# Optimization experiments

Hardware: AMD Instinct MI355X
Metric: run time of the kernel (lower is better)

The kernel has to match this reference:

```python
import jax, jax.numpy as jnp
import numpy as np

B, L, N = 512, 512, 128


def setup_inputs() -> dict:
    key = jax.random.key(0)
    k1, k2, k3, k4 = jax.random.split(key, 4)
    emission = jax.random.normal(k1, (B, L, N), dtype=jnp.float32)
    target = jax.random.randint(k2, (B, L), 0, N, dtype=jnp.int32)
    mask = jnp.ones((B, L), dtype=jnp.float32)
    # params: uniform(-0.1, 0.1) as in reset_parameters
    start_trans = jax.random.uniform(k3, (N,), minval=-0.1, maxval=0.1, dtype=jnp.float32)
    trans = jax.random.uniform(k4, (N, N), minval=-0.1, maxval=0.1, dtype=jnp.float32)
    return {"emission": emission, "target": target, "mask": mask,
            "start_trans": start_trans, "trans": trans}


def _normalizer(emission, mask, start_trans, trans):
    # scores: [B, N]
    scores0 = start_trans + emission[:, 0]
    em_t = jnp.swapaxes(emission, 0, 1)[1:]          # [L-1, B, N]
    m_t = jnp.swapaxes(mask, 0, 1)[1:, :, None]      # [L-1, B, 1]

    def step(scores, xs):
        em_i, m_i = xs
        nxt = jax.nn.logsumexp(scores[:, :, None] + trans[None], axis=1) + em_i
        nxt = m_i * nxt + (1.0 - m_i) * scores
        return nxt, None

    final, _ = jax.lax.scan(step, scores0, (em_t, m_t))
    return jax.nn.logsumexp(final, axis=1)            # [B]


def _path_score(emission, target, mask, start_trans, trans):
    # mask*next + (1-mask)*scores == scores + mask*increment -> fully vectorizable
    b = jnp.arange(emission.shape[0])
    t0 = target[:, 0]
    s0 = start_trans[t0] + emission[b, 0, t0]                         # [B]
    prev, cur = target[:, :-1], target[:, 1:]                         # [B, L-1]
    em_gather = jnp.take_along_axis(emission[:, 1:], cur[:, :, None], axis=2)[..., 0]
    inc = trans[prev, cur] + em_gather                                # [B, L-1]
    return s0 + jnp.sum(mask[:, 1:] * inc, axis=1)                    # [B]


def reference(emission, target, mask, start_trans, trans):
    path_scores = _path_score(emission, target, mask, start_trans, trans)
    normalizer = _normalizer(emission, mask, start_trans, trans)
    return jnp.mean(normalizer - path_scores)
```

## Files before the change

kernel.cpp:

```cpp
#include <hip/hip_runtime.h>

#define B_ 512
#define L_ 512
#define N_ 128
#define TM 256
#define C_BIAS 3.0f

typedef _Float16 h2_t __attribute__((ext_vector_type(2)));
typedef _Float16 h8_t __attribute__((ext_vector_type(8)));
typedef float    f4_t __attribute__((ext_vector_type(4)));

#define DPP_STEP_MAX(v, ctrl)                                                   \
    {                                                                           \
        int _t = __builtin_amdgcn_update_dpp(__float_as_int(v),                 \
                    __float_as_int(v), ctrl, 0xf, 0xf, false);                  \
        v = fmaxf(v, __int_as_float(_t));                                       \
    }
#define DPP_STEP_ADD(v, ctrl)                                                   \
    {                                                                           \
        int _t = __builtin_amdgcn_update_dpp(__float_as_int(v),                 \
                    __float_as_int(v), ctrl, 0xf, 0xf, false);                  \
        v = v + __int_as_float(_t);                                             \
    }

__device__ __forceinline__ float wave_max(float v) {
    DPP_STEP_MAX(v, 0xB1);
    DPP_STEP_MAX(v, 0x4E);
    DPP_STEP_MAX(v, 0x141);
    DPP_STEP_MAX(v, 0x140);
    DPP_STEP_MAX(v, 0x142);
    DPP_STEP_MAX(v, 0x143);
    return __int_as_float(__builtin_amdgcn_readlane(__float_as_int(v), 63));
}
__device__ __forceinline__ float wave_sum(float v) {
    DPP_STEP_ADD(v, 0xB1);
    DPP_STEP_ADD(v, 0x4E);
    DPP_STEP_ADD(v, 0x141);
    DPP_STEP_ADD(v, 0x140);
    DPP_STEP_ADD(v, 0x142);
    DPP_STEP_ADD(v, 0x143);
    return __int_as_float(__builtin_amdgcn_readlane(__float_as_int(v), 63));
}

#define CHAIN4(qv, BT)                                                          \
    f4_t qv = __builtin_amdgcn_mfma_f32_16x16x32_f16(A0, BT[0], z, 0, 0, 0);    \
    qv = __builtin_amdgcn_mfma_f32_16x16x32_f16(A1, BT[1], qv, 0, 0, 0);        \
    qv = __builtin_amdgcn_mfma_f32_16x16x32_f16(A2, BT[2], qv, 0, 0, 0);        \
    qv = __builtin_amdgcn_mfma_f32_16x16x32_f16(A3, BT[3], qv, 0, 0, 0);

__global__ __launch_bounds__(64, 1) void norm_kernel(
    const float* __restrict__ em, const int* __restrict__ tg,
    const float* __restrict__ mask, const float* __restrict__ st,
    const float* __restrict__ trans,
    float* __restrict__ alpha, float* __restrict__ beta,
    float* __restrict__ pathf, float* __restrict__ pathb)
{
    __shared__ __align__(16) _Float16 Eh[128];
    __shared__ float Mlds[TM];

    const int l  = threadIdx.x;
    const int c  = l & 15;
    const int h  = l >> 4;
    const int s0 = 32 * h + c;
    const int s1 = s0 + 16;
    const bool hb0 = (h & 1) != 0;
    const bool hb1 = (h & 2) != 0;
    const int b  = blockIdx.x >> 1;
    const int bw = blockIdx.x & 1;
    const size_t base = (size_t)b * L_ * N_;
    const int bL = b * L_;

    if (bw == 0) {
        float pacc = 0.f;
        for (int t = 1 + l; t < TM; t += 64) {
            int cur  = tg[bL + t];
            int prev = tg[bL + t - 1];
            pacc += mask[bL + t] * (trans[prev * N_ + cur] + em[base + (size_t)t * N_ + cur]);
        }
        pacc = wave_sum(pacc);
        if (l == 0) {
            int t0 = tg[bL];
            pathf[b] = pacc + st[t0] + em[base + t0];
        }

#pragma unroll
        for (int k = 0; k < 4; ++k) Mlds[l + 64 * k] = mask[bL + l + 64 * k];

        h8_t Bf[8][4];
#pragma unroll
        for (int jt = 0; jt < 8; ++jt)
#pragma unroll
            for (int ks = 0; ks < 4; ++ks) {
                h8_t f;
#pragma unroll
                for (int e = 0; e < 8; ++e)
                    f[e] = (_Float16)__expf(trans[(32 * ks + 8 * h + e) * N_ + 16 * jt + c]);
                Bf[jt][ks] = f;
            }

        float ns0 = st[s0] + em[base + s0];
        float ns1 = st[s1] + em[base + s1];
        float Mprev = wave_max(fmaxf(ns0, ns1));
        Eh[s0] = (_Float16)__expf(ns0 - Mprev - C_BIAS);
        Eh[s1] = (_Float16)__expf(ns1 - Mprev - C_BIAS);

        float pa0 = em[base + (size_t)1 * N_ + s0], pb0 = em[base + (size_t)1 * N_ + s1];
        float pa1 = em[base + (size_t)2 * N_ + s0], pb1 = em[base + (size_t)2 * N_ + s1];
        float pa2 = em[base + (size_t)3 * N_ + s0], pb2 = em[base + (size_t)3 * N_ + s1];
        float pa3 = em[base + (size_t)4 * N_ + s0], pb3 = em[base + (size_t)4 * N_ + s1];

        auto step = [&](int t, float& sa, float& sb) {
            float emv0 = sa, emv1 = sb;
            int tpf = t + 4; if (tpf > TM - 1) tpf = TM - 1;
            sa = em[base + (size_t)tpf * N_ + s0];
            sb = em[base + (size_t)tpf * N_ + s1];
            float mk = Mlds[t];

            float mx = wave_max(fmaxf(ns0, ns1));

            const _Float16* Eb = (const _Float16*)Eh;
            h8_t A0 = *(const h8_t*)(Eb + 8 * h);
            h8_t A1 = *(const h8_t*)(Eb + 32 + 8 * h);
            h8_t A2 = *(const h8_t*)(Eb + 64 + 8 * h);
            h8_t A3 = *(const h8_t*)(Eb + 96 + 8 * h);

            f4_t z = {0.f, 0.f, 0.f, 0.f};
            CHAIN4(q0, Bf[0]) CHAIN4(q1, Bf[1]) CHAIN4(q2, Bf[2]) CHAIN4(q3, Bf[3])
            CHAIN4(q4, Bf[4]) CHAIN4(q5, Bf[5]) CHAIN4(q6, Bf[6]) CHAIN4(q7, Bf[7])

            float sv0 = hb1 ? (hb0 ? q6[0] : q4[0]) : (hb0 ? q2[0] : q0[0]);
            float sv1 = hb1 ? (hb0 ? q7[0] : q5[0]) : (hb0 ? q3[0] : q1[0]);

            float badd = Mprev + C_BIAS;
            float nxt0 = __logf(sv0) + badd + emv0;
            float nxt1 = __logf(sv1) + badd + emv1;
            float im = 1.f - mk;
            ns0 = mk * nxt0 + im * ns0;
            ns1 = mk * nxt1 + im * ns1;

            Mprev = mx;
            Eh[s0] = (_Float16)__expf(ns0 - mx - C_BIAS);
            Eh[s1] = (_Float16)__expf(ns1 - mx - C_BIAS);
        };

        for (int tt = 1; tt + 3 < TM; tt += 4) {
            step(tt    , pa0, pb0);
            step(tt + 1, pa1, pb1);
            step(tt + 2, pa2, pb2);
            step(tt + 3, pa3, pb3);
        }
        step(TM - 3, pa0, pb0);
        step(TM - 2, pa1, pb1);
        step(TM - 1, pa2, pb2);

        alpha[b * N_ + s0] = ns0;
        alpha[b * N_ + s1] = ns1;
    } else {
        float pacc = 0.f;
        for (int t = TM + l; t < L_; t += 64) {
            int cur  = tg[bL + t];
            int prev = tg[bL + t - 1];
            pacc += mask[bL + t] * (trans[prev * N_ + cur] + em[base + (size_t)t * N_ + cur]);
        }
        pacc = wave_sum(pacc);
        if (l == 0) pathb[b] = pacc;

#pragma unroll
        for (int k = 0; k < 4; ++k) Mlds[l + 64 * k] = mask[bL + TM + l + 64 * k];

        h8_t Bf[8][4];
#pragma unroll
        for (int it = 0; it < 8; ++it)
#pragma unroll
            for (int ks = 0; ks < 4; ++ks) {
                const float* p = trans + (size_t)(16 * it + c) * N_ + 32 * ks + 8 * h;
                float4 q0 = *(const float4*)p;
                float4 q1 = *(const float4*)(p + 4);
                h8_t f;
                f[0] = (_Float16)__expf(q0.x); f[1] = (_Float16)__expf(q0.y);
                f[2] = (_Float16)__expf(q0.z); f[3] = (_Float16)__expf(q0.w);
                f[4] = (_Float16)__expf(q1.x); f[5] = (_Float16)__expf(q1.y);
                f[6] = (_Float16)__expf(q1.z); f[7] = (_Float16)__expf(q1.w);
                Bf[it][ks] = f;
            }

        float b0 = 0.f, b1 = 0.f;
        float v0 = em[base + (size_t)(L_ - 1) * N_ + s0];
        float v1 = em[base + (size_t)(L_ - 1) * N_ + s1];
        float Mprev = wave_max(fmaxf(v0, v1));
        Eh[s0] = (_Float16)__expf(v0 - Mprev - C_BIAS);
        Eh[s1] = (_Float16)__expf(v1 - Mprev - C_BIAS);

        float pa0 = em[base + (size_t)510 * N_ + s0], pb0 = em[base + (size_t)510 * N_ + s1];
        float pa1 = em[base + (size_t)509 * N_ + s0], pb1 = em[base + (size_t)509 * N_ + s1];
        float pa2 = em[base + (size_t)508 * N_ + s0], pb2 = em[base + (size_t)508 * N_ + s1];
        float pa3 = em[base + (size_t)507 * N_ + s0], pb3 = em[base + (size_t)507 * N_ + s1];

        auto step = [&](int t, float& sa, float& sb) {
            float emt0 = sa, emt1 = sb;
            int tpf = t - 4; if (tpf < TM - 1) tpf = TM - 1;
            sa = em[base + (size_t)tpf * N_ + s0];
            sb = em[base + (size_t)tpf * N_ + s1];
            float mk = Mlds[t + 1 - TM];

            float mx = wave_max(fmaxf(v0, v1));

            const _Float16* Fb = (const _Float16*)Eh;
            h8_t A0 = *(const h8_t*)(Fb + 8 * h);
            h8_t A1 = *(const h8_t*)(Fb + 32 + 8 * h);
            h8_t A2 = *(const h8_t*)(Fb + 64 + 8 * h);
            h8_t A3 = *(const h8_t*)(Fb + 96 + 8 * h);

            f4_t z = {0.f, 0.f, 0.f, 0.f};
            CHAIN4(q0, Bf[0]) CHAIN4(q1, Bf[1]) CHAIN4(q2, Bf[2]) CHAIN4(q3, Bf[3])
            CHAIN4(q4, Bf[4]) CHAIN4(q5, Bf[5]) CHAIN4(q6, Bf[6]) CHAIN4(q7, Bf[7])

            float sv0 = hb1 ? (hb0 ? q6[0] : q4[0]) : (hb0 ? q2[0] : q0[0]);
            float sv1 = hb1 ? (hb0 ? q7[0] : q5[0]) : (hb0 ? q3[0] : q1[0]);

            float badd = Mprev + C_BIAS;
            float upd0 = __logf(sv0) + badd;
            float upd1 = __logf(sv1) + badd;
            float im = 1.f - mk;
            b0 = mk * upd0 + im * b0;
            b1 = mk * upd1 + im * b1;

            v0 = b0 + emt0;
            v1 = b1 + emt1;
            Mprev = mx;
            Eh[s0] = (_Float16)__expf(v0 - mx - C_BIAS);
            Eh[s1] = (_Float16)__expf(v1 - mx - C_BIAS);
        };

        for (int tt = 510; tt >= 258; tt -= 4) {
            step(tt    , pa0, pb0);
            step(tt - 1, pa1, pb1);
            step(tt - 2, pa2, pb2);
            step(tt - 3, pa3, pb3);
        }

        beta[b * N_ + s0] = b0;
        beta[b * N_ + s1] = b1;
    }
}

__global__ __launch_bounds__(64) void zres_kernel(
    const float* __restrict__ alpha, const float* __restrict__ beta,
    const float* __restrict__ pathf, const float* __restrict__ pathb,
    float* __restrict__ zres)
{
    const int l = threadIdx.x;
    const int b = blockIdx.x;
    float2 av = *(const float2*)(alpha + b * N_ + 2 * l);
    float2 bv = *(const float2*)(beta  + b * N_ + 2 * l);
    float v0 = av.x + bv.x;
    float v1 = av.y + bv.y;
    float m = wave_max(fmaxf(v0, v1));
    float s = wave_sum(__expf(v0 - m) + __expf(v1 - m));
    if (l == 0) zres[b] = m + __logf(s) - pathf[b] - pathb[b];
}

__global__ __launch_bounds__(64) void mean_kernel(
    const float* __restrict__ zres, float* __restrict__ out)
{
    const int l = threadIdx.x;
    const float4* z4 = (const float4*)zres;
    float4 a = z4[2 * l];
    float4 c = z4[2 * l + 1];
    float acc = ((a.x + a.y) + (a.z + a.w)) + ((c.x + c.y) + (c.z + c.w));
    acc = wave_sum(acc);
    if (l == 0) out[0] = acc * (1.0f / (float)B_);
}

extern "C" void kernel_launch(void* const* d_in, const int* in_sizes, int n_in,
                              void* d_out, int out_size, void* d_ws, size_t ws_size,
                              hipStream_t stream) {
    const float* emission    = (const float*)d_in[0];
    const int*   target      = (const int*)  d_in[1];
    const float* mask        = (const float*)d_in[2];
    const float* start_trans = (const float*)d_in[3];
    const float* trans       = (const float*)d_in[4];
    float* out = (float*)d_out;

    float* ws_f  = (float*)d_ws;
    float* alpha = ws_f;
    float* beta  = ws_f + B_ * N_;
    float* pathf = ws_f + 2 * B_ * N_;
    float* pathb = ws_f + 2 * B_ * N_ + B_;
    float* zres  = ws_f + 2 * B_ * N_ + 2 * B_;

    norm_kernel<<<2 * B_, 64, 0, stream>>>(emission, target, mask, start_trans,
                                           trans, alpha, beta, pathf, pathb);
    zres_kernel<<<B_, 64, 0, stream>>>(alpha, beta, pathf, pathb, zres);
    mean_kernel<<<1, 64, 0, stream>>>(zres, out);
}
```

Measured before the change: 307.7 us.

## Switch CRF recurrence matmul from fp16 MFMA chains to scaled FP8 MFMA

Replaces the four chained fp16 16x16x32 MFMAs per output tile with a single scaled 16x16x128 FP8 (e4m3) MFMA. The exp(trans) matrix and the per-step exp-scores vector are quantized to FP8 with unit scales. This shortens the serial per-timestep latency chain of the latency-bound recurrence, and also shrinks the register-held B fragments and the LDS vector. The cost is much lower precision in the exponentiated scores (3 mantissa bits, and small values get flushed or become subnormal), which risks accuracy error in the normalizer over 511 steps.

```diff
diff --git a/kernel.cpp b/kernel.cpp
--- a/kernel.cpp
+++ b/kernel.cpp
@@ -6,9 +6,8 @@
 #define TM 256
 #define C_BIAS 3.0f
 
-typedef _Float16 h2_t __attribute__((ext_vector_type(2)));
-typedef _Float16 h8_t __attribute__((ext_vector_type(8)));
-typedef float    f4_t __attribute__((ext_vector_type(4)));
+typedef float f4_t __attribute__((ext_vector_type(4)));
+typedef int   v8i_t __attribute__((ext_vector_type(8)));
 
 #define DPP_STEP_MAX(v, ctrl)                                                   \
     {                                                                           \
@@ -42,11 +41,44 @@
     return __int_as_float(__builtin_amdgcn_readlane(__float_as_int(v), 63));
 }
 
-#define CHAIN4(qv, BT)                                                          \
-    f4_t qv = __builtin_amdgcn_mfma_f32_16x16x32_f16(A0, BT[0], z, 0, 0, 0);    \
-    qv = __builtin_amdgcn_mfma_f32_16x16x32_f16(A1, BT[1], qv, 0, 0, 0);        \
-    qv = __builtin_amdgcn_mfma_f32_16x16x32_f16(A2, BT[2], qv, 0, 0, 0);        \
-    qv = __builtin_amdgcn_mfma_f32_16x16x32_f16(A3, BT[3], qv, 0, 0, 0);
+#if __has_builtin(__builtin_amdgcn_cvt_pk_fp8_f32)
+__device__ __forceinline__ unsigned fp8_pair(float a, float b) {
+    return (unsigned)__builtin_amdgcn_cvt_pk_fp8_f32(a, b, 0, false);
+}
+__device__ __forceinline__ unsigned fp8_quad(float a, float b, float c, float d) {
+    int lo = __builtin_amdgcn_cvt_pk_fp8_f32(a, b, 0, false);
+    return (unsigned)__builtin_amdgcn_cvt_pk_fp8_f32(c, d, lo, true);
+}
+#else
+__device__ __forceinline__ unsigned char f32_e4m3(float v) {
+    if (!(v > 0.f)) return 0;
+    if (v >= 448.f) return 0x7E;
+    if (v < 0.015625f) {
+        int m = (int)(v * 512.f + 0.5f);
+        return (unsigned char)m;
+    }
+    union { float f; unsigned u; } x; x.f = v;
+    unsigned u = x.u;
+    unsigned lsb = (u >> 20) & 1;
+    u += 0x0007FFFF + lsb;
+    int e = (int)((u >> 23) & 255) - 127 + 7;
+    unsigned m = (u >> 20) & 7;
+    if (e > 15) return 0x7E;
+    return (unsigned char)((e << 3) | m);
+}
+__device__ __forceinline__ unsigned fp8_pair(float a, float b) {
+    return (unsigned)f32_e4m3(a) | ((unsigned)f32_e4m3(b) << 8);
+}
+__device__ __forceinline__ unsigned fp8_quad(float a, float b, float c, float d) {
+    return fp8_pair(a, b) | (fp8_pair(c, d) << 16);
+}
+#endif
+
+#define SCALE_ONE 0x7F7F7F7F
+
+#define MXMFMA(qv, bt)                                                          \
+    f4_t qv = __builtin_amdgcn_mfma_scale_f32_16x16x128_f8f6f4(                 \
+        Afrag, bt, z, 0, 0, 0, SCALE_ONE, 0, SCALE_ONE);
 
 __global__ __launch_bounds__(64, 1) void norm_kernel(
     const float* __restrict__ em, const int* __restrict__ tg,
@@ -55,7 +87,7 @@
     float* __restrict__ alpha, float* __restrict__ beta,
     float* __restrict__ pathf, float* __restrict__ pathb)
 {
-    __shared__ __align__(16) _Float16 Eh[128];
+    __shared__ __align__(32) unsigned char Eh[128];
     __shared__ float Mlds[TM];
 
     const int l  = threadIdx.x;
@@ -86,23 +118,30 @@
 #pragma unroll
         for (int k = 0; k < 4; ++k) Mlds[l + 64 * k] = mask[bL + l + 64 * k];
 
-        h8_t Bf[8][4];
-#pragma unroll
-        for (int jt = 0; jt < 8; ++jt)
-#pragma unroll
-            for (int ks = 0; ks < 4; ++ks) {
-                h8_t f;
-#pragma unroll
-                for (int e = 0; e < 8; ++e)
-                    f[e] = (_Float16)__expf(trans[(32 * ks + 8 * h + e) * N_ + 16 * jt + c]);
-                Bf[jt][ks] = f;
+        v8i_t Bf[8];
+#pragma unroll
+        for (int jt = 0; jt < 8; ++jt) {
+            v8i_t bb;
+#pragma unroll
+            for (int dd = 0; dd < 8; ++dd) {
+                const float* p = trans + (size_t)(32 * h + 4 * dd) * N_ + 16 * jt + c;
+                float f0 = __expf(p[0]);
+                float f1 = __expf(p[N_]);
+                float f2 = __expf(p[2 * N_]);
+                float f3 = __expf(p[3 * N_]);
+                bb[dd] = (int)fp8_quad(f0, f1, f2, f3);
             }
+            Bf[jt] = bb;
+        }
 
         float ns0 = st[s0] + em[base + s0];
         float ns1 = st[s1] + em[base + s1];
         float Mprev = wave_max(fmaxf(ns0, ns1));
-        Eh[s0] = (_Float16)__expf(ns0 - Mprev - C_BIAS);
-        Eh[s1] = (_Float16)__expf(ns1 - Mprev - C_BIAS);
+        {
+            unsigned p = fp8_pair(__expf(ns0 - Mprev - C_BIAS), __expf(ns1 - Mprev - C_BIAS));
+            Eh[s0] = (unsigned char)(p & 0xFF);
+            Eh[s1] = (unsigned char)((p >> 8) & 0xFF);
+        }
 
         float pa0 = em[base + (size_t)1 * N_ + s0], pb0 = em[base + (size_t)1 * N_ + s1];
         float pa1 = em[base + (size_t)2 * N_ + s0], pb1 = em[base + (size_t)2 * N_ + s1];
@@ -118,15 +157,11 @@
 
             float mx = wave_max(fmaxf(ns0, ns1));
 
-            const _Float16* Eb = (const _Float16*)Eh;
-            h8_t A0 = *(const h8_t*)(Eb + 8 * h);
-            h8_t A1 = *(const h8_t*)(Eb + 32 + 8 * h);
-            h8_t A2 = *(const h8_t*)(Eb + 64 + 8 * h);
-            h8_t A3 = *(const h8_t*)(Eb + 96 + 8 * h);
+            v8i_t Afrag = *(const v8i_t*)(Eh + 32 * h);
 
             f4_t z = {0.f, 0.f, 0.f, 0.f};
-            CHAIN4(q0, Bf[0]) CHAIN4(q1, Bf[1]) CHAIN4(q2, Bf[2]) CHAIN4(q3, Bf[3])
-            CHAIN4(q4, Bf[4]) CHAIN4(q5, Bf[5]) CHAIN4(q6, Bf[6]) CHAIN4(q7, Bf[7])
+            MXMFMA(q0, Bf[0]) MXMFMA(q1, Bf[1]) MXMFMA(q2, Bf[2]) MXMFMA(q3, Bf[3])
+            MXMFMA(q4, Bf[4]) MXMFMA(q5, Bf[5]) MXMFMA(q6, Bf[6]) MXMFMA(q7, Bf[7])
 
             float sv0 = hb1 ? (hb0 ? q6[0] : q4[0]) : (hb0 ? q2[0] : q0[0]);
             float sv1 = hb1 ? (hb0 ? q7[0] : q5[0]) : (hb0 ? q3[0] : q1[0]);
@@ -139,8 +174,9 @@
             ns1 = mk * nxt1 + im * ns1;
 
             Mprev = mx;
-            Eh[s0] = (_Float16)__expf(ns0 - mx - C_BIAS);
-            Eh[s1] = (_Float16)__expf(ns1 - mx - C_BIAS);
+            unsigned p = fp8_pair(__expf(ns0 - mx - C_BIAS), __expf(ns1 - mx - C_BIAS));
+            Eh[s0] = (unsigned char)(p & 0xFF);
+            Eh[s1] = (unsigned char)((p >> 8) & 0xFF);
         };
 
         for (int tt = 1; tt + 3 < TM; tt += 4) {
@@ -168,28 +204,27 @@
 #pragma unroll
         for (int k = 0; k < 4; ++k) Mlds[l + 64 * k] = mask[bL + TM + l + 64 * k];
 
-        h8_t Bf[8][4];
-#pragma unroll
-        for (int it = 0; it < 8; ++it)
-#pragma unroll
-            for (int ks = 0; ks < 4; ++ks) {
-                const float* p = trans + (size_t)(16 * it + c) * N_ + 32 * ks + 8 * h;
-                float4 q0 = *(const float4*)p;
-                float4 q1 = *(const float4*)(p + 4);
-                h8_t f;
-                f[0] = (_Float16)__expf(q0.x); f[1] = (_Float16)__expf(q0.y);
-                f[2] = (_Float16)__expf(q0.z); f[3] = (_Float16)__expf(q0.w);
-                f[4] = (_Float16)__expf(q1.x); f[5] = (_Float16)__expf(q1.y);
-                f[6] = (_Float16)__expf(q1.z); f[7] = (_Float16)__expf(q1.w);
-                Bf[it][ks] = f;
+        v8i_t Bf[8];
+#pragma unroll
+        for (int it = 0; it < 8; ++it) {
+            v8i_t bb;
+#pragma unroll
+            for (int dd = 0; dd < 8; ++dd) {
+                float4 q = *(const float4*)(trans + (size_t)(16 * it + c) * N_ + 32 * h + 4 * dd);
+                bb[dd] = (int)fp8_quad(__expf(q.x), __expf(q.y), __expf(q.z), __expf(q.w));
             }
+            Bf[it] = bb;
+        }
 
         float b0 = 0.f, b1 = 0.f;
         float v0 = em[base + (size_t)(L_ - 1) * N_ + s0];
         float v1 = em[base + (size_t)(L_ - 1) * N_ + s1];
         float Mprev = wave_max(fmaxf(v0, v1));
-        Eh[s0] = (_Float16)__expf(v0 - Mprev - C_BIAS);
-        Eh[s1] = (_Float16)__expf(v1 - Mprev - C_BIAS);
+        {
+            unsigned p = fp8_pair(__expf(v0 - Mprev - C_BIAS), __expf(v1 - Mprev - C_BIAS));
+            Eh[s0] = (unsigned char)(p & 0xFF);
+            Eh[s1] = (unsigned char)((p >> 8) & 0xFF);
+        }
 
         float pa0 = em[base + (size_t)510 * N_ + s0], pb0 = em[base + (size_t)510 * N_ + s1];
         float pa1 = em[base + (size_t)509 * N_ + s0], pb1 = em[base + (size_t)509 * N_ + s1];
@@ -205,15 +240,11 @@
 
             float mx = wave_max(fmaxf(v0, v1));
 
-            const _Float16* Fb = (const _Float16*)Eh;
-            h8_t A0 = *(const h8_t*)(Fb + 8 * h);
-            h8_t A1 = *(const h8_t*)(Fb + 32 + 8 * h);
-            h8_t A2 = *(const h8_t*)(Fb + 64 + 8 * h);
-            h8_t A3 = *(const h8_t*)(Fb + 96 + 8 * h);
+            v8i_t Afrag = *(const v8i_t*)(Eh + 32 * h);
 
             f4_t z = {0.f, 0.f, 0.f, 0.f};
-            CHAIN4(q0, Bf[0]) CHAIN4(q1, Bf[1]) CHAIN4(q2, Bf[2]) CHAIN4(q3, Bf[3])
-            CHAIN4(q4, Bf[4]) CHAIN4(q5, Bf[5]) CHAIN4(q6, Bf[6]) CHAIN4(q7, Bf[7])
+            MXMFMA(q0, Bf[0]) MXMFMA(q1, Bf[1]) MXMFMA(q2, Bf[2]) MXMFMA(q3, Bf[3])
+            MXMFMA(q4, Bf[4]) MXMFMA(q5, Bf[5]) MXMFMA(q6, Bf[6]) MXMFMA(q7, Bf[7])
 
             float sv0 = hb1 ? (hb0 ? q6[0] : q4[0]) : (hb0 ? q2[0] : q0[0]);
             float sv1 = hb1 ? (hb0 ? q7[0] : q5[0]) : (hb0 ? q3[0] : q1[0]);
@@ -228,8 +259,9 @@
             v0 = b0 + emt0;
             v1 = b1 + emt1;
             Mprev = mx;
-            Eh[s0] = (_Float16)__expf(v0 - mx - C_BIAS);
-            Eh[s1] = (_Float16)__expf(v1 - mx - C_BIAS);
+            unsigned p = fp8_pair(__expf(v0 - mx - C_BIAS), __expf(v1 - mx - C_BIAS));
+            Eh[s0] = (unsigned char)(p & 0xFF);
+            Eh[s1] = (unsigned char)((p >> 8) & 0xFF);
         };
 
         for (int tt = 510; tt >= 258; tt -= 4) {
```

Result: faster. 279.9 us (-9.0%).
